# Kernel optimization log

Hardware: AMD Instinct MI355X
Metric: run time of the kernel (lower is better)

Reference implementation:

```python
import jax, jax.numpy as jnp
import numpy as np

TEMPERATURE = 0.5  # init kwarg: temperature
EPS = 1e-8         # torch CosineSimilarity eps


def setup_inputs() -> dict:
    key = jax.random.key(0)
    k1, k2 = jax.random.split(key)
    B, D = 2048, 256
    return {
        "z_i": jax.random.normal(k1, (B, D), dtype=jnp.float32),
        "z_j": jax.random.normal(k2, (B, D), dtype=jnp.float32),
    }


def reference(z_i, z_j):
    # NT-Xent (SimCLR) loss, world_size = 1.
    B = z_i.shape[0]
    N = 2 * B
    z = jnp.concatenate([z_i, z_j], axis=0)                       # [N, D]
    # Cosine similarity = normalized dot product (fused normalize + matmul,
    # avoiding the torch broadcast NxNxD intermediate).
    zn = z / jnp.clip(jnp.linalg.norm(z, axis=1, keepdims=True), EPS)
    sim = (zn @ zn.T) / TEMPERATURE                               # [N, N]
    # Positive pair similarity for each row: diag offsets +B and -B.
    pos = jnp.concatenate([jnp.diagonal(sim, offset=B),
                           jnp.diagonal(sim, offset=-B)], axis=0)  # [N]
    # CrossEntropy with label 0 over logits [pos, negatives] equals
    # -pos + logsumexp over {pos} U negatives = all off-diagonal entries,
    # since the mask removes exactly the diagonal and the positive pair
    # (which is re-added as `pos`). Mask diagonal with -inf.
    neg_inf = jnp.finfo(sim.dtype).min
    sim_masked = jnp.where(jnp.eye(N, dtype=bool), neg_inf, sim)
    lse = jax.scipy.special.logsumexp(sim_masked, axis=1)          # [N]
    # reduction='sum' then / N  ->  mean over rows
    loss = jnp.sum(lse - pos) / N
    return loss
```

## Files before the change

kernel.cpp:

```cpp
#include <hip/hip_runtime.h>


#define NROWS 4096
#define DDIM 256
#define BHALF 2048
#define TILE 128
#define BK 64
#define LDP 72
#define NCB (NROWS / TILE)
#define INV_T 2.0f

typedef short bf16x8 __attribute__((ext_vector_type(8)));
typedef float f32x4 __attribute__((ext_vector_type(4)));

__device__ inline unsigned short f2bf(float f) {
    union { float f; unsigned u; } c; c.f = f;
    unsigned u = c.u + 0x7fffu + ((c.u >> 16) & 1u);
    return (unsigned short)(u >> 16);
}

__global__ __launch_bounds__(256) void k_normalize(
    const float* __restrict__ zi, const float* __restrict__ zj,
    unsigned short* __restrict__ zn) {
    const int wave = threadIdx.x >> 6, lane = threadIdx.x & 63;
    const int row = blockIdx.x * 4 + wave;
    const float* src = (row < BHALF) ? (zi + row * DDIM)
                                     : (zj + (row - BHALF) * DDIM);
    const float4 v = ((const float4*)src)[lane];
    float ss = v.x * v.x + v.y * v.y + v.z * v.z + v.w * v.w;
    #pragma unroll
    for (int m = 1; m < 64; m <<= 1) ss += __shfl_xor(ss, m);
    const float scale = 1.0f / fmaxf(sqrtf(ss), 1e-8f);
    ushort4 o;
    o.x = f2bf(v.x * scale); o.y = f2bf(v.y * scale);
    o.z = f2bf(v.z * scale); o.w = f2bf(v.w * scale);
    ((ushort4*)(zn + row * DDIM))[lane] = o;
}

__global__ __launch_bounds__(256) void k_simlse(
    const unsigned short* __restrict__ zn,
    float* __restrict__ partial,
    float* __restrict__ posv) {
    __shared__ unsigned short As[TILE * LDP];
    __shared__ unsigned short Bs[TILE * LDP];
    __shared__ float pscratch[TILE];
    __shared__ float cscratch[TILE];

    int t = blockIdx.x, bx = 0, rem = NCB;
    while (t >= rem) { t -= rem; ++bx; --rem; }
    const int by = bx + t;

    const int tid = threadIdx.x;
    const int wave = tid >> 6, lane = tid & 63;
    const int quad = lane >> 4, l15 = lane & 15;
    const int wr = wave >> 1, wc = wave & 1;
    const int rowBase = bx * TILE;
    const int colBase = by * TILE;

    f32x4 acc[4][4] = {};

    #pragma unroll
    for (int kb = 0; kb < DDIM / BK; ++kb) {
        __syncthreads();
        #pragma unroll
        for (int i = 0; i < 4; ++i) {
            const int flat = tid + i * 256;
            const int r = flat >> 3, c = flat & 7;
            *(bf16x8*)&As[r * LDP + c * 8] =
                *(const bf16x8*)&zn[(rowBase + r) * DDIM + kb * BK + c * 8];
            *(bf16x8*)&Bs[r * LDP + c * 8] =
                *(const bf16x8*)&zn[(colBase + r) * DDIM + kb * BK + c * 8];
        }
        __syncthreads();
        #pragma unroll
        for (int s = 0; s < 2; ++s) {
            bf16x8 af[4], bf[4];
            #pragma unroll
            for (int mt = 0; mt < 4; ++mt)
                af[mt] = *(const bf16x8*)&As[(wr * 64 + mt * 16 + l15) * LDP + s * 32 + quad * 8];
            #pragma unroll
            for (int nt = 0; nt < 4; ++nt)
                bf[nt] = *(const bf16x8*)&Bs[(wc * 64 + nt * 16 + l15) * LDP + s * 32 + quad * 8];
            #pragma unroll
            for (int mt = 0; mt < 4; ++mt)
                #pragma unroll
                for (int nt = 0; nt < 4; ++nt)
                    acc[mt][nt] = __builtin_amdgcn_mfma_f32_16x16x32_bf16(
                        af[mt], bf[nt], acc[mt][nt], 0, 0, 0);
        }
    }

    float rsum[4][4];
    float csum[4] = {};
    #pragma unroll
    for (int mt = 0; mt < 4; ++mt) {
        #pragma unroll
        for (int r = 0; r < 4; ++r) {
            const int grow = rowBase + wr * 64 + mt * 16 + quad * 4 + r;
            float s = 0.f;
            #pragma unroll
            for (int nt = 0; nt < 4; ++nt) {
                const int gcol = colBase + wc * 64 + nt * 16 + l15;
                const float simv = acc[mt][nt][r] * INV_T;
                const float e = (gcol != grow) ? __expf(simv) : 0.f;
                s += e;
                csum[nt] += e;
                if (gcol == grow + BHALF) {
                    posv[grow] = simv;
                    posv[gcol] = simv;
                }
            }
            s += __shfl_xor(s, 1); s += __shfl_xor(s, 2);
            s += __shfl_xor(s, 4); s += __shfl_xor(s, 8);
            rsum[mt][r] = s;
        }
    }
    #pragma unroll
    for (int nt = 0; nt < 4; ++nt) {
        csum[nt] += __shfl_xor(csum[nt], 16);
        csum[nt] += __shfl_xor(csum[nt], 32);
    }

    __syncthreads();
    if (wc == 0 && l15 == 0) {
        #pragma unroll
        for (int mt = 0; mt < 4; ++mt)
            #pragma unroll
            for (int r = 0; r < 4; ++r)
                pscratch[wr * 64 + mt * 16 + quad * 4 + r] = rsum[mt][r];
    }
    if (wr == 0 && quad == 0) {
        #pragma unroll
        for (int nt = 0; nt < 4; ++nt)
            cscratch[wc * 64 + nt * 16 + l15] = csum[nt];
    }
    __syncthreads();
    if (wc == 1 && l15 == 0) {
        #pragma unroll
        for (int mt = 0; mt < 4; ++mt)
            #pragma unroll
            for (int r = 0; r < 4; ++r) {
                const int lr = wr * 64 + mt * 16 + quad * 4 + r;
                partial[by * NROWS + rowBase + lr] = rsum[mt][r] + pscratch[lr];
            }
    }
    if (bx != by && wr == 1 && quad == 0) {
        #pragma unroll
        for (int nt = 0; nt < 4; ++nt) {
            const int lc = wc * 64 + nt * 16 + l15;
            partial[bx * NROWS + colBase + lc] = csum[nt] + cscratch[lc];
        }
    }
}

__global__ __launch_bounds__(256) void k_rowlse(
    const float* __restrict__ partial, const float* __restrict__ posv,
    float* __restrict__ blocksum) {
    __shared__ float red[4];
    const int tid = threadIdx.x;
    const int row = blockIdx.x * 256 + tid;
    float s = 0.f;
    #pragma unroll
    for (int p = 0; p < NCB; ++p) s += partial[p * NROWS + row];
    float v = __logf(s) - posv[row];
    #pragma unroll
    for (int m = 1; m < 64; m <<= 1) v += __shfl_xor(v, m);
    if ((tid & 63) == 0) red[tid >> 6] = v;
    __syncthreads();
    if (tid == 0)
        blocksum[blockIdx.x] = red[0] + red[1] + red[2] + red[3];
}

__global__ __launch_bounds__(64) void k_final2(
    const float* __restrict__ blocksum, float* __restrict__ out) {
    const int lane = threadIdx.x;
    float v = (lane < 16) ? blocksum[lane] : 0.f;
    #pragma unroll
    for (int m = 1; m < 16; m <<= 1) v += __shfl_xor(v, m);
    if (lane == 0) out[0] = v * (1.0f / (float)NROWS);
}

extern "C" void kernel_launch(void* const* d_in, const int* in_sizes, int n_in,
                              void* d_out, int out_size, void* d_ws, size_t ws_size,
                              hipStream_t stream) {
    const float* zi = (const float*)d_in[0];
    const float* zj = (const float*)d_in[1];
    float* out = (float*)d_out;

    unsigned short* zn = (unsigned short*)d_ws;
    float* partial = (float*)((char*)d_ws + NROWS * DDIM * 2);
    float* posv = partial + NCB * NROWS;
    float* blocksum = posv + NROWS;

    k_normalize<<<NROWS / 4, 256, 0, stream>>>(zi, zj, zn);
    k_simlse<<<NCB * (NCB + 1) / 2, 256, 0, stream>>>(zn, partial, posv);
    k_rowlse<<<16, 256, 0, stream>>>(partial, posv, blocksum);
    k_final2<<<1, 64, 0, stream>>>(blocksum, out);
}
```

Measured before the change: 80.09 us.

## Fuse normalization into the similarity kernel and merge the final reductions

Measured after the change: 125.0 us. 56.1% more time.

```diff
diff --git a/kernel.cpp b/kernel.cpp
--- a/kernel.cpp
+++ b/kernel.cpp
@@ -7,44 +7,26 @@
 #define TILE 128
 #define BK 64
 #define LDP 72
-#define NCB (NROWS / TILE)
+#define NCB 32
 #define INV_T 2.0f
 
 typedef short bf16x8 __attribute__((ext_vector_type(8)));
 typedef float f32x4 __attribute__((ext_vector_type(4)));
 
-__device__ inline unsigned short f2bf(float f) {
-    union { float f; unsigned u; } c; c.f = f;
-    unsigned u = c.u + 0x7fffu + ((c.u >> 16) & 1u);
-    return (unsigned short)(u >> 16);
-}
-
-__global__ __launch_bounds__(256) void k_normalize(
+__device__ inline unsigned bfpack(float lo, float hi) {
+    union { float f; unsigned u; } a, b;
+    a.f = lo; b.f = hi;
+    return __builtin_amdgcn_perm(b.u + 0x8000u, a.u + 0x8000u, 0x07060302u);
+}
+
+__global__ __launch_bounds__(256) void k_simlse(
     const float* __restrict__ zi, const float* __restrict__ zj,
-    unsigned short* __restrict__ zn) {
-    const int wave = threadIdx.x >> 6, lane = threadIdx.x & 63;
-    const int row = blockIdx.x * 4 + wave;
-    const float* src = (row < BHALF) ? (zi + row * DDIM)
-                                     : (zj + (row - BHALF) * DDIM);
-    const float4 v = ((const float4*)src)[lane];
-    float ss = v.x * v.x + v.y * v.y + v.z * v.z + v.w * v.w;
-    #pragma unroll
-    for (int m = 1; m < 64; m <<= 1) ss += __shfl_xor(ss, m);
-    const float scale = 1.0f / fmaxf(sqrtf(ss), 1e-8f);
-    ushort4 o;
-    o.x = f2bf(v.x * scale); o.y = f2bf(v.y * scale);
-    o.z = f2bf(v.z * scale); o.w = f2bf(v.w * scale);
-    ((ushort4*)(zn + row * DDIM))[lane] = o;
-}
-
-__global__ __launch_bounds__(256) void k_simlse(
-    const unsigned short* __restrict__ zn,
     float* __restrict__ partial,
     float* __restrict__ posv) {
     __shared__ unsigned short As[TILE * LDP];
     __shared__ unsigned short Bs[TILE * LDP];
-    __shared__ float pscratch[TILE];
-    __shared__ float cscratch[TILE];
+    __shared__ float rnA[TILE], rnB[TILE];
+    __shared__ float pscratch[TILE], cscratch[TILE];
 
     int t = blockIdx.x, bx = 0, rem = NCB;
     while (t >= rem) { t -= rem; ++bx; --rem; }
@@ -56,7 +38,13 @@
     const int wr = wave >> 1, wc = wave & 1;
     const int rowBase = bx * TILE;
     const int colBase = by * TILE;
-
+    const float* srcA = (bx < 16) ? (zi + rowBase * DDIM)
+                                  : (zj + (rowBase - BHALF) * DDIM);
+    const float* srcB = (by < 16) ? (zi + colBase * DDIM)
+                                  : (zj + (colBase - BHALF) * DDIM);
+
+    const int c8 = tid & 7;
+    float sqA[4] = {}, sqB[4] = {};
     f32x4 acc[4][4] = {};
 
     #pragma unroll
@@ -64,12 +52,21 @@
         __syncthreads();
         #pragma unroll
         for (int i = 0; i < 4; ++i) {
-            const int flat = tid + i * 256;
-            const int r = flat >> 3, c = flat & 7;
-            *(bf16x8*)&As[r * LDP + c * 8] =
-                *(const bf16x8*)&zn[(rowBase + r) * DDIM + kb * BK + c * 8];
-            *(bf16x8*)&Bs[r * LDP + c * 8] =
-                *(const bf16x8*)&zn[(colBase + r) * DDIM + kb * BK + c * 8];
+            const int r = (tid >> 3) + i * 32;
+            const float* pa = srcA + r * DDIM + kb * BK + c8 * 8;
+            const float* pb = srcB + r * DDIM + kb * BK + c8 * 8;
+            const float4 a0 = *(const float4*)pa, a1 = *(const float4*)(pa + 4);
+            const float4 b0 = *(const float4*)pb, b1 = *(const float4*)(pb + 4);
+            sqA[i] += a0.x*a0.x + a0.y*a0.y + a0.z*a0.z + a0.w*a0.w
+                    + a1.x*a1.x + a1.y*a1.y + a1.z*a1.z + a1.w*a1.w;
+            sqB[i] += b0.x*b0.x + b0.y*b0.y + b0.z*b0.z + b0.w*b0.w
+                    + b1.x*b1.x + b1.y*b1.y + b1.z*b1.z + b1.w*b1.w;
+            uint4 pkA = { bfpack(a0.x,a0.y), bfpack(a0.z,a0.w),
+                          bfpack(a1.x,a1.y), bfpack(a1.z,a1.w) };
+            uint4 pkB = { bfpack(b0.x,b0.y), bfpack(b0.z,b0.w),
+                          bfpack(b1.x,b1.y), bfpack(b1.z,b1.w) };
+            *(uint4*)&As[r * LDP + c8 * 8] = pkA;
+            *(uint4*)&Bs[r * LDP + c8 * 8] = pkB;
         }
         __syncthreads();
         #pragma unroll
@@ -90,6 +87,28 @@
         }
     }
 
+    #pragma unroll
+    for (int i = 0; i < 4; ++i) {
+        float a = sqA[i], b = sqB[i];
+        a += __shfl_xor(a, 1); a += __shfl_xor(a, 2); a += __shfl_xor(a, 4);
+        b += __shfl_xor(b, 1); b += __shfl_xor(b, 2); b += __shfl_xor(b, 4);
+        if (c8 == 0) {
+            const int r = (tid >> 3) + i * 32;
+            rnA[r] = 1.0f / fmaxf(sqrtf(a), 1e-8f);
+            rnB[r] = 1.0f / fmaxf(sqrtf(b), 1e-8f);
+        }
+    }
+    __syncthreads();
+
+    f32x4 rna[4];
+    float rnb[4];
+    #pragma unroll
+    for (int mt = 0; mt < 4; ++mt)
+        rna[mt] = *(const f32x4*)&rnA[wr * 64 + mt * 16 + quad * 4];
+    #pragma unroll
+    for (int nt = 0; nt < 4; ++nt)
+        rnb[nt] = rnB[wc * 64 + nt * 16 + l15];
+
     float rsum[4][4];
     float csum[4] = {};
     #pragma unroll
@@ -101,7 +120,7 @@
             #pragma unroll
             for (int nt = 0; nt < 4; ++nt) {
                 const int gcol = colBase + wc * 64 + nt * 16 + l15;
-                const float simv = acc[mt][nt][r] * INV_T;
+                const float simv = acc[mt][nt][r] * rna[mt][r] * rnb[nt] * INV_T;
                 const float e = (gcol != grow) ? __expf(simv) : 0.f;
                 s += e;
                 csum[nt] += e;
@@ -153,31 +172,30 @@
     }
 }
 
-__global__ __launch_bounds__(256) void k_rowlse(
+__global__ __launch_bounds__(1024) void k_finalize(
     const float* __restrict__ partial, const float* __restrict__ posv,
-    float* __restrict__ blocksum) {
-    __shared__ float red[4];
+    float* __restrict__ out) {
+    __shared__ float red[16];
     const int tid = threadIdx.x;
-    const int row = blockIdx.x * 256 + tid;
-    float s = 0.f;
-    #pragma unroll
-    for (int p = 0; p < NCB; ++p) s += partial[p * NROWS + row];
-    float v = __logf(s) - posv[row];
-    #pragma unroll
-    for (int m = 1; m < 64; m <<= 1) v += __shfl_xor(v, m);
-    if ((tid & 63) == 0) red[tid >> 6] = v;
-    __syncthreads();
-    if (tid == 0)
-        blocksum[blockIdx.x] = red[0] + red[1] + red[2] + red[3];
-}
-
-__global__ __launch_bounds__(64) void k_final2(
-    const float* __restrict__ blocksum, float* __restrict__ out) {
-    const int lane = threadIdx.x;
-    float v = (lane < 16) ? blocksum[lane] : 0.f;
-    #pragma unroll
-    for (int m = 1; m < 16; m <<= 1) v += __shfl_xor(v, m);
-    if (lane == 0) out[0] = v * (1.0f / (float)NROWS);
+    float acc = 0.f;
+    #pragma unroll
+    for (int rr = 0; rr < 4; ++rr) {
+        const int row = tid + rr * 1024;
+        float s = 0.f;
+        #pragma unroll
+        for (int p = 0; p < NCB; ++p) s += partial[p * NROWS + row];
+        acc += __logf(s) - posv[row];
+    }
+    #pragma unroll
+    for (int m = 1; m < 64; m <<= 1) acc += __shfl_xor(acc, m);
+    if ((tid & 63) == 0) red[tid >> 6] = acc;
+    __syncthreads();
+    if (tid < 64) {
+        float v = (tid < 16) ? red[tid] : 0.f;
+        #pragma unroll
+        for (int m = 1; m < 16; m <<= 1) v += __shfl_xor(v, m);
+        if (tid == 0) out[0] = v * (1.0f / (float)NROWS);
+    }
 }
 
 extern "C" void kernel_launch(void* const* d_in, const int* in_sizes, int n_in,
@@ -187,13 +205,9 @@
     const float* zj = (const float*)d_in[1];
     float* out = (float*)d_out;
 
-    unsigned short* zn = (unsigned short*)d_ws;
-    float* partial = (float*)((char*)d_ws + NROWS * DDIM * 2);
+    float* partial = (float*)d_ws;
     float* posv = partial + NCB * NROWS;
-    float* blocksum = posv + NROWS;
-
-    k_normalize<<<NROWS / 4, 256, 0, stream>>>(zi, zj, zn);
-    k_simlse<<<NCB * (NCB + 1) / 2, 256, 0, stream>>>(zn, partial, posv);
-    k_rowlse<<<16, 256, 0, stream>>>(partial, posv, blocksum);
-    k_final2<<<1, 64, 0, stream>>>(blocksum, out);
-}
+
+    k_simlse<<<NCB * (NCB + 1) / 2, 256, 0, stream>>>(zi, zj, partial, posv);
+    k_finalize<<<1, 1024, 0, stream>>>(partial, posv, out);
+}
```
